# Performance work log

Measured on AMD Instinct MI355X. Metric: run time of the kernel, lower is better.

## Reference

```python
import math
import jax, jax.numpy as jnp
import numpy as np

H = 1024        # hidden_size
NH = 16         # num_attention_heads
HD = H // NH    # attention_head_size
I = 4096        # intermediate_size
B, S = 4, 2048
LN_EPS = 1e-5


def setup_inputs() -> dict:
    key = jax.random.key(0)
    ks = jax.random.split(key, 12)
    s = 0.02
    return {
        "x": jax.random.normal(ks[0], (B, S, H), dtype=jnp.float32),
        "ln1_g": jnp.ones((H,), jnp.float32),
        "ln1_b": jnp.zeros((H,), jnp.float32),
        "qkv_w": jax.random.normal(ks[1], (H, 3 * H), jnp.float32) * s,
        "qkv_b": jnp.zeros((3 * H,), jnp.float32),
        "out_w": jax.random.normal(ks[2], (H, H), jnp.float32) * s,
        "out_b": jnp.zeros((H,), jnp.float32),
        "ln2_g": jnp.ones((H,), jnp.float32),
        "ln2_b": jnp.zeros((H,), jnp.float32),
        "w1": jax.random.normal(ks[3], (H, I), jnp.float32) * s,
        "b1": jnp.zeros((I,), jnp.float32),
        "w2": jax.random.normal(ks[4], (I, H), jnp.float32) * s,
        "b2": jnp.zeros((H,), jnp.float32),
    }


def _layernorm(x, g, b):
    mu = jnp.mean(x, axis=-1, keepdims=True)
    var = jnp.mean(jnp.square(x - mu), axis=-1, keepdims=True)
    return (x - mu) * jax.lax.rsqrt(var + LN_EPS) * g + b


def _gelu_tanh(x):
    c = math.sqrt(2.0 / math.pi)
    return 0.5 * x * (1.0 + jnp.tanh(c * (x + 0.044715 * x * x * x)))


def reference(x, ln1_g, ln1_b, qkv_w, qkv_b, out_w, out_b, ln2_g, ln2_b, w1, b1, w2, b2):
    b, s, _ = x.shape
    h = _layernorm(x, ln1_g, ln1_b)
    qkv = h @ qkv_w + qkv_b                      # [B,S,3H]
    q, k, v = jnp.split(qkv, 3, axis=-1)
    # [B,S,H] -> [B,NH,S,HD]
    def heads(t):
        return t.reshape(b, s, NH, HD).transpose(0, 2, 1, 3)
    q, k, v = heads(q), heads(k), heads(v)
    scores = jnp.einsum("bhqd,bhkd->bhqk", q, k) / math.sqrt(HD)
    probs = jax.nn.softmax(scores, axis=-1)
    attn = jnp.einsum("bhqk,bhkd->bhqd", probs, v)
    attn = attn.transpose(0, 2, 1, 3).reshape(b, s, H)
    attn = attn @ out_w + out_b
    x = x + attn
    h2 = _layernorm(x, ln2_g, ln2_b)
    mlp = _gelu_tanh(h2 @ w1 + b1) @ w2 + b2
    x = x + mlp
    return x
```

## Files before the change

### kernel.cpp

```cpp
#include <hip/hip_runtime.h>
#include <math.h>

#define H 1024
#define NHEAD 16
#define HDIM 64
#define IDIM 4096
#define BATCH 4
#define SEQ 2048
#define NTOK 8192
#define LN_EPS 1e-5f

typedef __bf16 bf16x8 __attribute__((ext_vector_type(8)));
typedef __bf16 bf16x4 __attribute__((ext_vector_type(4)));
typedef float f32x4 __attribute__((ext_vector_type(4)));
typedef unsigned short ushort8 __attribute__((ext_vector_type(8)));
typedef unsigned short ushort4v __attribute__((ext_vector_type(4)));

__device__ __forceinline__ unsigned short f2bf(float f) {
  union { float f; unsigned int u; } v; v.f = f;
  unsigned int u = v.u;
  return (unsigned short)((u + 0x7FFFu + ((u >> 16) & 1u)) >> 16);
}

__global__ void transpose_cast_kernel(const float* __restrict__ W,
                                      unsigned short* __restrict__ Wt,
                                      int K, int N) {
  __shared__ unsigned short tile[32][33];
  int n0 = blockIdx.x * 32, k0 = blockIdx.y * 32;
  int tx = threadIdx.x, ty = threadIdx.y;
#pragma unroll
  for (int i = 0; i < 4; i++) {
    int k = ty + i * 8;
    tile[tx][k] = f2bf(W[(size_t)(k0 + k) * N + n0 + tx]);
  }
  __syncthreads();
#pragma unroll
  for (int i = 0; i < 4; i++) {
    int n = ty + i * 8;
    Wt[(size_t)(n0 + n) * K + k0 + tx] = tile[n][tx];
  }
}

__global__ void transpose_v_kernel(const unsigned short* __restrict__ qkv,
                                   unsigned short* __restrict__ vt) {
  __shared__ unsigned short tile[32][33];
  int s0 = blockIdx.x * 32, d0 = blockIdx.y * 32;
  int bh = blockIdx.z, b = bh >> 4, h = bh & 15;
  int tx = threadIdx.x, ty = threadIdx.y;
#pragma unroll
  for (int i = 0; i < 4; i++) {
    int s = ty + i * 8;
    tile[s][tx] = qkv[((size_t)b * SEQ + s0 + s) * (3 * H) + 2 * H + h * HDIM + d0 + tx];
  }
  __syncthreads();
#pragma unroll
  for (int i = 0; i < 4; i++) {
    int d = ty + i * 8;
    vt[((size_t)bh * HDIM + d0 + d) * SEQ + s0 + tx] = tile[tx][d];
  }
}

__global__ __launch_bounds__(256)
void layernorm_kernel(const float* __restrict__ x, const float* __restrict__ g,
                      const float* __restrict__ b, unsigned short* __restrict__ out) {
  __shared__ float sb[4];
  int row = blockIdx.x;
  int tid = threadIdx.x;
  const float4* xr = (const float4*)(x + (size_t)row * H);
  float4 v = xr[tid];
  float s = v.x + v.y + v.z + v.w;
#pragma unroll
  for (int o = 32; o > 0; o >>= 1) s += __shfl_down(s, o);
  if ((tid & 63) == 0) sb[tid >> 6] = s;
  __syncthreads();
  float mu = (sb[0] + sb[1] + sb[2] + sb[3]) * (1.0f / H);
  __syncthreads();
  float dx = v.x - mu, dy = v.y - mu, dz = v.z - mu, dw = v.w - mu;
  float s2 = dx * dx + dy * dy + dz * dz + dw * dw;
#pragma unroll
  for (int o = 32; o > 0; o >>= 1) s2 += __shfl_down(s2, o);
  if ((tid & 63) == 0) sb[tid >> 6] = s2;
  __syncthreads();
  float var = (sb[0] + sb[1] + sb[2] + sb[3]) * (1.0f / H);
  float rs = rsqrtf(var + LN_EPS);
  float4 gv = ((const float4*)g)[tid];
  float4 bv = ((const float4*)b)[tid];
  ushort4v ov;
  ov[0] = f2bf(dx * rs * gv.x + bv.x);
  ov[1] = f2bf(dy * rs * gv.y + bv.y);
  ov[2] = f2bf(dz * rs * gv.z + bv.z);
  ov[3] = f2bf(dw * rs * gv.w + bv.w);
  ((ushort4v*)(out + (size_t)row * H))[tid] = ov;
}

template <int EPI>
__global__ __launch_bounds__(256)
void gemm_bt_kernel(const unsigned short* __restrict__ A,
                    const unsigned short* __restrict__ Bt,
                    const float* __restrict__ bias,
                    const float* __restrict__ res,
                    void* __restrict__ out, int M, int N, int K) {
  __shared__ __align__(16) unsigned short As[128 * 32];
  __shared__ __align__(16) unsigned short Bs[128 * 32];
  int tid = threadIdx.x;
  int wave = tid >> 6, lane = tid & 63;
  int quad = lane >> 4, l16 = lane & 15;
  int wm = wave >> 1, wn = wave & 1;
  int m0 = blockIdx.y * 128, n0 = blockIdx.x * 128;
  f32x4 acc[4][4];
#pragma unroll
  for (int i = 0; i < 4; i++)
#pragma unroll
    for (int j = 0; j < 4; j++) acc[i][j] = (f32x4){0.f, 0.f, 0.f, 0.f};

  int rl = (lane >> 2);
  int cphys = lane & 3;
  for (int k0 = 0; k0 < K; k0 += 32) {
    __syncthreads();
#pragma unroll
    for (int t = 0; t < 2; t++) {
      int ch = wave * 2 + t;
      int rloc = ch * 16 + rl;
      int clog = cphys ^ ((rloc >> 1) & 3);
      const unsigned short* ga = A + (size_t)(m0 + rloc) * K + k0 + clog * 8;
      __builtin_amdgcn_global_load_lds(
          (const __attribute__((address_space(1))) unsigned int*)ga,
          (__attribute__((address_space(3))) unsigned int*)(As + ch * 512), 16, 0, 0);
      const unsigned short* gb = Bt + (size_t)(n0 + rloc) * K + k0 + clog * 8;
      __builtin_amdgcn_global_load_lds(
          (const __attribute__((address_space(1))) unsigned int*)gb,
          (__attribute__((address_space(3))) unsigned int*)(Bs + ch * 512), 16, 0, 0);
    }
    __syncthreads();
    bf16x8 af[4], bfv[4];
#pragma unroll
    for (int i = 0; i < 4; i++) {
      int ra = wm * 64 + i * 16 + l16;
      af[i] = *(const bf16x8*)&As[ra * 32 + ((quad ^ ((ra >> 1) & 3)) << 3)];
      int rb = wn * 64 + i * 16 + l16;
      bfv[i] = *(const bf16x8*)&Bs[rb * 32 + ((quad ^ ((rb >> 1) & 3)) << 3)];
    }
#pragma unroll
    for (int i = 0; i < 4; i++)
#pragma unroll
      for (int j = 0; j < 4; j++)
        acc[i][j] = __builtin_amdgcn_mfma_f32_16x16x32_bf16(bfv[j], af[i], acc[i][j], 0, 0, 0);
  }
#pragma unroll
  for (int i = 0; i < 4; i++) {
    int m = m0 + wm * 64 + i * 16 + l16;
#pragma unroll
    for (int j = 0; j < 4; j++) {
      int nb = n0 + wn * 64 + j * 16 + quad * 4;
      float4 bv4 = *(const float4*)&bias[nb];
      float v0 = acc[i][j][0] + bv4.x;
      float v1 = acc[i][j][1] + bv4.y;
      float v2 = acc[i][j][2] + bv4.z;
      float v3 = acc[i][j][3] + bv4.w;
      size_t off = (size_t)m * N + nb;
      if (EPI == 0) {
        bf16x4 pk = {(__bf16)v0, (__bf16)v1, (__bf16)v2, (__bf16)v3};
        *(bf16x4*)&((unsigned short*)out)[off] = pk;
      } else if (EPI == 1) {
        float g0 = v0 / (1.f + __expf(-1.5957691216057308f * (v0 + 0.044715f * v0 * v0 * v0)));
        float g1 = v1 / (1.f + __expf(-1.5957691216057308f * (v1 + 0.044715f * v1 * v1 * v1)));
        float g2 = v2 / (1.f + __expf(-1.5957691216057308f * (v2 + 0.044715f * v2 * v2 * v2)));
        float g3 = v3 / (1.f + __expf(-1.5957691216057308f * (v3 + 0.044715f * v3 * v3 * v3)));
        bf16x4 pk = {(__bf16)g0, (__bf16)g1, (__bf16)g2, (__bf16)g3};
        *(bf16x4*)&((unsigned short*)out)[off] = pk;
      } else {
        float4 rv = *(const float4*)&res[off];
        float4 o4;
        o4.x = v0 + rv.x; o4.y = v1 + rv.y; o4.z = v2 + rv.z; o4.w = v3 + rv.w;
        *(float4*)&((float*)out)[off] = o4;
      }
    }
  }
}

__global__ __launch_bounds__(256)
void flash_attn_kernel(const unsigned short* __restrict__ qkv,
                       const unsigned short* __restrict__ vt,
                       unsigned short* __restrict__ attn_out) {
  constexpr int LPs = 72;
  __shared__ __align__(16) unsigned short Ks[64 * 64];
  __shared__ __align__(16) unsigned short Ps[4 * 32 * LPs];
  int tid = threadIdx.x;
  int wave = tid >> 6, lane = tid & 63;
  int quad = lane >> 4, l16 = lane & 15;
  int bh = blockIdx.y, b = bh >> 4, h = bh & 15;
  int qblk = blockIdx.x * 128 + wave * 32;
  const size_t qrow = 3 * H;
  const size_t tok0 = (size_t)b * SEQ;
  const size_t vbase = (size_t)bh * HDIM * SEQ;
  unsigned short* Psw = Ps + wave * 32 * LPs;

  bf16x8 qb[2][2];
#pragma unroll
  for (int mb = 0; mb < 2; mb++)
#pragma unroll
    for (int ks = 0; ks < 2; ks++)
      qb[mb][ks] = *(const bf16x8*)&qkv[(tok0 + qblk + mb * 16 + l16) * qrow +
                                        h * HDIM + ks * 32 + quad * 8];

  float l_part[2] = {0.f, 0.f};
  f32x4 o_acc[2][4];
#pragma unroll
  for (int mb = 0; mb < 2; mb++)
#pragma unroll
    for (int db = 0; db < 4; db++) o_acc[mb][db] = (f32x4){0.f, 0.f, 0.f, 0.f};

  int srow = lane >> 3;
  int schunk = (lane & 7) ^ srow;

  for (int kv0 = 0; kv0 < SEQ; kv0 += 64) {
    __syncthreads();
#pragma unroll
    for (int t = 0; t < 2; t++) {
      int rbase = wave * 16 + t * 8;
      const unsigned short* ga =
          &qkv[(tok0 + kv0 + rbase + srow) * qrow + H + h * HDIM + schunk * 8];
      __builtin_amdgcn_global_load_lds(
          (const __attribute__((address_space(1))) unsigned int*)ga,
          (__attribute__((address_space(3))) unsigned int*)(Ks + rbase * 64), 16, 0, 0);
    }
    bf16x8 va[4][2];
#pragma unroll
    for (int db = 0; db < 4; db++)
#pragma unroll
      for (int ks = 0; ks < 2; ks++)
        va[db][ks] = *(const bf16x8*)&vt[vbase + (size_t)(db * 16 + l16) * SEQ +
                                         kv0 + ks * 32 + quad * 8];
    __syncthreads();
#pragma unroll
    for (int nb = 0; nb < 4; nb++) {
      int row = nb * 16 + l16;
      bf16x8 ka[2];
#pragma unroll
      for (int ks = 0; ks < 2; ks++) {
        int pc = (ks * 4 + quad) ^ (row & 7);
        ka[ks] = *(const bf16x8*)&Ks[row * 64 + pc * 8];
      }
      f32x4 st[2];
#pragma unroll
      for (int mb = 0; mb < 2; mb++) st[mb] = (f32x4){0.f, 0.f, 0.f, 0.f};
#pragma unroll
      for (int ks = 0; ks < 2; ks++)
#pragma unroll
        for (int mb = 0; mb < 2; mb++)
          st[mb] = __builtin_amdgcn_mfma_f32_16x16x32_bf16(ka[ks], qb[mb][ks], st[mb], 0, 0, 0);
#pragma unroll
      for (int mb = 0; mb < 2; mb++) {
        float p0 = __expf(st[mb][0] * 0.125f);
        float p1 = __expf(st[mb][1] * 0.125f);
        float p2 = __expf(st[mb][2] * 0.125f);
        float p3 = __expf(st[mb][3] * 0.125f);
        l_part[mb] += (p0 + p1) + (p2 + p3);
        bf16x4 pk = {(__bf16)p0, (__bf16)p1, (__bf16)p2, (__bf16)p3};
        *(bf16x4*)&Psw[(mb * 16 + l16) * LPs + nb * 16 + quad * 4] = pk;
      }
    }
    __asm__ volatile("s_waitcnt lgkmcnt(0)" ::: "memory");
#pragma unroll
    for (int ks = 0; ks < 2; ks++) {
      bf16x8 pb[2];
#pragma unroll
      for (int mb = 0; mb < 2; mb++)
        pb[mb] = *(const bf16x8*)&Psw[(mb * 16 + l16) * LPs + ks * 32 + quad * 8];
#pragma unroll
      for (int db = 0; db < 4; db++)
#pragma unroll
        for (int mb = 0; mb < 2; mb++)
          o_acc[mb][db] = __builtin_amdgcn_mfma_f32_16x16x32_bf16(va[db][ks], pb[mb],
                                                                  o_acc[mb][db], 0, 0, 0);
    }
  }
#pragma unroll
  for (int mb = 0; mb < 2; mb++) {
    l_part[mb] += __shfl_xor(l_part[mb], 16);
    l_part[mb] += __shfl_xor(l_part[mb], 32);
    l_part[mb] = 1.0f / l_part[mb];
  }
#pragma unroll
  for (int mb = 0; mb < 2; mb++) {
#pragma unroll
    for (int db = 0; db < 4; db++) {
      ushort4v o;
#pragma unroll
      for (int r = 0; r < 4; r++) o[r] = f2bf(o_acc[mb][db][r] * l_part[mb]);
      *(ushort4v*)&attn_out[(tok0 + qblk + mb * 16 + l16) * H + h * HDIM +
                            db * 16 + quad * 4] = o;
    }
  }
}

extern "C" void kernel_launch(void* const* d_in, const int* in_sizes, int n_in,
                              void* d_out, int out_size, void* d_ws, size_t ws_size,
                              hipStream_t stream) {
  const float* x = (const float*)d_in[0];
  const float* ln1_g = (const float*)d_in[1];
  const float* ln1_b = (const float*)d_in[2];
  const float* qkv_w = (const float*)d_in[3];
  const float* qkv_b = (const float*)d_in[4];
  const float* out_w = (const float*)d_in[5];
  const float* out_b = (const float*)d_in[6];
  const float* ln2_g = (const float*)d_in[7];
  const float* ln2_b = (const float*)d_in[8];
  const float* w1 = (const float*)d_in[9];
  const float* b1 = (const float*)d_in[10];
  const float* w2 = (const float*)d_in[11];
  const float* b2 = (const float*)d_in[12];
  float* outp = (float*)d_out;

  size_t off = 0;
  auto take = [&](size_t n) {
    char* p = (char*)d_ws + off;
    off += (n + 255) & ~(size_t)255;
    return p;
  };
  unsigned short* h1 = (unsigned short*)take((size_t)NTOK * H * 2);
  unsigned short* qkvb = (unsigned short*)take((size_t)NTOK * 3 * H * 2);
  unsigned short* attn = (unsigned short*)take((size_t)NTOK * H * 2);
  float* x1 = (float*)take((size_t)NTOK * H * 4);
  unsigned short* qkvwt = (unsigned short*)take((size_t)3 * H * H * 2);
  unsigned short* outwt = (unsigned short*)take((size_t)H * H * 2);
  unsigned short* w1t = (unsigned short*)take((size_t)H * IDIM * 2);
  unsigned short* w2t = (unsigned short*)take((size_t)H * IDIM * 2);
  unsigned short* h2 = h1;
  unsigned short* mid = qkvb;
  unsigned short* vt = (unsigned short*)x1;

  dim3 tb(32, 8);
  transpose_cast_kernel<<<dim3(3 * H / 32, H / 32), tb, 0, stream>>>(qkv_w, qkvwt, H, 3 * H);
  transpose_cast_kernel<<<dim3(H / 32, H / 32), tb, 0, stream>>>(out_w, outwt, H, H);
  transpose_cast_kernel<<<dim3(IDIM / 32, H / 32), tb, 0, stream>>>(w1, w1t, H, IDIM);
  transpose_cast_kernel<<<dim3(H / 32, IDIM / 32), tb, 0, stream>>>(w2, w2t, IDIM, H);

  layernorm_kernel<<<NTOK, 256, 0, stream>>>(x, ln1_g, ln1_b, h1);
  gemm_bt_kernel<0><<<dim3(3 * H / 128, NTOK / 128), 256, 0, stream>>>(
      h1, qkvwt, qkv_b, nullptr, qkvb, NTOK, 3 * H, H);
  transpose_v_kernel<<<dim3(SEQ / 32, HDIM / 32, BATCH * NHEAD), tb, 0, stream>>>(qkvb, vt);
  flash_attn_kernel<<<dim3(SEQ / 128, BATCH * NHEAD), 256, 0, stream>>>(qkvb, vt, attn);
  gemm_bt_kernel<2><<<dim3(H / 128, NTOK / 128), 256, 0, stream>>>(
      attn, outwt, out_b, x, x1, NTOK, H, H);
  layernorm_kernel<<<NTOK, 256, 0, stream>>>(x1, ln2_g, ln2_b, h2);
  gemm_bt_kernel<1><<<dim3(IDIM / 128, NTOK / 128), 256, 0, stream>>>(
      h2, w1t, b1, nullptr, mid, NTOK, IDIM, H);
  gemm_bt_kernel<2><<<dim3(H / 128, NTOK / 128), 256, 0, stream>>>(
      mid, w2t, b2, x1, outp, NTOK, H, IDIM);
}
```

Before: 696.4 us.

## Fuse V transpose into QKV GEMM epilogue and double-buffer K tiles in attention

The QKV GEMM epilogue now writes the V slice straight into the transposed per-head layout, so the separate transpose_v kernel and its extra read and write of V go away. The flash attention kernel double-buffers its K tiles in LDS, prefetching the next tile with async global-to-LDS loads while the current one is computed, and drops one barrier per iteration. It also splits the P·V step into two halves interleaved with the score computation. In exchange, the V epilogue issues scattered 2-byte stores with a stride of SEQ, and the attention kernel uses twice the K shared memory.

```diff
diff --git a/kernel.cpp b/kernel.cpp
--- a/kernel.cpp
+++ b/kernel.cpp
@@ -38,25 +38,6 @@
   for (int i = 0; i < 4; i++) {
     int n = ty + i * 8;
     Wt[(size_t)(n0 + n) * K + k0 + tx] = tile[n][tx];
-  }
-}
-
-__global__ void transpose_v_kernel(const unsigned short* __restrict__ qkv,
-                                   unsigned short* __restrict__ vt) {
-  __shared__ unsigned short tile[32][33];
-  int s0 = blockIdx.x * 32, d0 = blockIdx.y * 32;
-  int bh = blockIdx.z, b = bh >> 4, h = bh & 15;
-  int tx = threadIdx.x, ty = threadIdx.y;
-#pragma unroll
-  for (int i = 0; i < 4; i++) {
-    int s = ty + i * 8;
-    tile[s][tx] = qkv[((size_t)b * SEQ + s0 + s) * (3 * H) + 2 * H + h * HDIM + d0 + tx];
-  }
-  __syncthreads();
-#pragma unroll
-  for (int i = 0; i < 4; i++) {
-    int d = ty + i * 8;
-    vt[((size_t)bh * HDIM + d0 + d) * SEQ + s0 + tx] = tile[tx][d];
   }
 }
 
@@ -99,7 +80,8 @@
                     const unsigned short* __restrict__ Bt,
                     const float* __restrict__ bias,
                     const float* __restrict__ res,
-                    void* __restrict__ out, int M, int N, int K) {
+                    void* __restrict__ out, unsigned short* __restrict__ vt_out,
+                    int M, int N, int K) {
   __shared__ __align__(16) unsigned short As[128 * 32];
   __shared__ __align__(16) unsigned short Bs[128 * 32];
   int tid = threadIdx.x;
@@ -146,6 +128,7 @@
       for (int j = 0; j < 4; j++)
         acc[i][j] = __builtin_amdgcn_mfma_f32_16x16x32_bf16(bfv[j], af[i], acc[i][j], 0, 0, 0);
   }
+  bool vslice = (EPI == 0) && (vt_out != nullptr) && (n0 >= 2 * H);
 #pragma unroll
   for (int i = 0; i < 4; i++) {
     int m = m0 + wm * 64 + i * 16 + l16;
@@ -159,8 +142,19 @@
       float v3 = acc[i][j][3] + bv4.w;
       size_t off = (size_t)m * N + nb;
       if (EPI == 0) {
-        bf16x4 pk = {(__bf16)v0, (__bf16)v1, (__bf16)v2, (__bf16)v3};
-        *(bf16x4*)&((unsigned short*)out)[off] = pk;
+        if (vslice) {
+          int bb = m >> 11, s = m & (SEQ - 1);
+          int cb = nb - 2 * H;
+          int hh = cb >> 6, dd = cb & 63;
+          size_t base = ((size_t)(bb * NHEAD + hh) * HDIM + dd) * SEQ + s;
+          vt_out[base] = f2bf(v0);
+          vt_out[base + SEQ] = f2bf(v1);
+          vt_out[base + 2 * SEQ] = f2bf(v2);
+          vt_out[base + 3 * SEQ] = f2bf(v3);
+        } else {
+          bf16x4 pk = {(__bf16)v0, (__bf16)v1, (__bf16)v2, (__bf16)v3};
+          *(bf16x4*)&((unsigned short*)out)[off] = pk;
+        }
       } else if (EPI == 1) {
         float g0 = v0 / (1.f + __expf(-1.5957691216057308f * (v0 + 0.044715f * v0 * v0 * v0)));
         float g1 = v1 / (1.f + __expf(-1.5957691216057308f * (v1 + 0.044715f * v1 * v1 * v1)));
@@ -183,7 +177,7 @@
                        const unsigned short* __restrict__ vt,
                        unsigned short* __restrict__ attn_out) {
   constexpr int LPs = 72;
-  __shared__ __align__(16) unsigned short Ks[64 * 64];
+  __shared__ __align__(16) unsigned short Ks[2][64 * 64];
   __shared__ __align__(16) unsigned short Ps[4 * 32 * LPs];
   int tid = threadIdx.x;
   int wave = tid >> 6, lane = tid & 63;
@@ -213,17 +207,21 @@
   int srow = lane >> 3;
   int schunk = (lane & 7) ^ srow;
 
+#pragma unroll
+  for (int t = 0; t < 2; t++) {
+    int rbase = wave * 16 + t * 8;
+    const unsigned short* ga =
+        &qkv[(tok0 + rbase + srow) * qrow + H + h * HDIM + schunk * 8];
+    __builtin_amdgcn_global_load_lds(
+        (const __attribute__((address_space(1))) unsigned int*)ga,
+        (__attribute__((address_space(3))) unsigned int*)(&Ks[0][rbase * 64]), 16, 0, 0);
+  }
+
   for (int kv0 = 0; kv0 < SEQ; kv0 += 64) {
+    int buf = (kv0 >> 6) & 1;
+    const unsigned short* Kb = Ks[buf];
+    unsigned short* Kn = Ks[buf ^ 1];
     __syncthreads();
-#pragma unroll
-    for (int t = 0; t < 2; t++) {
-      int rbase = wave * 16 + t * 8;
-      const unsigned short* ga =
-          &qkv[(tok0 + kv0 + rbase + srow) * qrow + H + h * HDIM + schunk * 8];
-      __builtin_amdgcn_global_load_lds(
-          (const __attribute__((address_space(1))) unsigned int*)ga,
-          (__attribute__((address_space(3))) unsigned int*)(Ks + rbase * 64), 16, 0, 0);
-    }
     bf16x8 va[4][2];
 #pragma unroll
     for (int db = 0; db < 4; db++)
@@ -231,47 +229,58 @@
       for (int ks = 0; ks < 2; ks++)
         va[db][ks] = *(const bf16x8*)&vt[vbase + (size_t)(db * 16 + l16) * SEQ +
                                          kv0 + ks * 32 + quad * 8];
-    __syncthreads();
-#pragma unroll
-    for (int nb = 0; nb < 4; nb++) {
-      int row = nb * 16 + l16;
-      bf16x8 ka[2];
-#pragma unroll
-      for (int ks = 0; ks < 2; ks++) {
-        int pc = (ks * 4 + quad) ^ (row & 7);
-        ka[ks] = *(const bf16x8*)&Ks[row * 64 + pc * 8];
+    if (kv0 + 64 < SEQ) {
+#pragma unroll
+      for (int t = 0; t < 2; t++) {
+        int rbase = wave * 16 + t * 8;
+        const unsigned short* ga =
+            &qkv[(tok0 + kv0 + 64 + rbase + srow) * qrow + H + h * HDIM + schunk * 8];
+        __builtin_amdgcn_global_load_lds(
+            (const __attribute__((address_space(1))) unsigned int*)ga,
+            (__attribute__((address_space(3))) unsigned int*)(Kn + rbase * 64), 16, 0, 0);
       }
-      f32x4 st[2];
-#pragma unroll
-      for (int mb = 0; mb < 2; mb++) st[mb] = (f32x4){0.f, 0.f, 0.f, 0.f};
-#pragma unroll
-      for (int ks = 0; ks < 2; ks++)
+    }
+#pragma unroll
+    for (int half = 0; half < 2; half++) {
+#pragma unroll
+      for (int nbl = 0; nbl < 2; nbl++) {
+        int nb = half * 2 + nbl;
+        int row = nb * 16 + l16;
+        bf16x8 ka[2];
+#pragma unroll
+        for (int ks = 0; ks < 2; ks++) {
+          int pc = (ks * 4 + quad) ^ (row & 7);
+          ka[ks] = *(const bf16x8*)&Kb[row * 64 + pc * 8];
+        }
+        f32x4 st[2];
+#pragma unroll
+        for (int mb = 0; mb < 2; mb++) st[mb] = (f32x4){0.f, 0.f, 0.f, 0.f};
+#pragma unroll
+        for (int ks = 0; ks < 2; ks++)
+#pragma unroll
+          for (int mb = 0; mb < 2; mb++)
+            st[mb] = __builtin_amdgcn_mfma_f32_16x16x32_bf16(ka[ks], qb[mb][ks], st[mb], 0, 0, 0);
+#pragma unroll
+        for (int mb = 0; mb < 2; mb++) {
+          float p0 = __expf(st[mb][0] * 0.125f);
+          float p1 = __expf(st[mb][1] * 0.125f);
+          float p2 = __expf(st[mb][2] * 0.125f);
+          float p3 = __expf(st[mb][3] * 0.125f);
+          l_part[mb] += (p0 + p1) + (p2 + p3);
+          bf16x4 pk = {(__bf16)p0, (__bf16)p1, (__bf16)p2, (__bf16)p3};
+          *(bf16x4*)&Psw[(mb * 16 + l16) * LPs + nb * 16 + quad * 4] = pk;
+        }
+      }
+      __asm__ volatile("s_waitcnt lgkmcnt(0)" ::: "memory");
+      bf16x8 pb[2];
+#pragma unroll
+      for (int mb = 0; mb < 2; mb++)
+        pb[mb] = *(const bf16x8*)&Psw[(mb * 16 + l16) * LPs + half * 32 + quad * 8];
+#pragma unroll
+      for (int db = 0; db < 4; db++)
 #pragma unroll
         for (int mb = 0; mb < 2; mb++)
-          st[mb] = __builtin_amdgcn_mfma_f32_16x16x32_bf16(ka[ks], qb[mb][ks], st[mb], 0, 0, 0);
-#pragma unroll
-      for (int mb = 0; mb < 2; mb++) {
-        float p0 = __expf(st[mb][0] * 0.125f);
-        float p1 = __expf(st[mb][1] * 0.125f);
-        float p2 = __expf(st[mb][2] * 0.125f);
-        float p3 = __expf(st[mb][3] * 0.125f);
-        l_part[mb] += (p0 + p1) + (p2 + p3);
-        bf16x4 pk = {(__bf16)p0, (__bf16)p1, (__bf16)p2, (__bf16)p3};
-        *(bf16x4*)&Psw[(mb * 16 + l16) * LPs + nb * 16 + quad * 4] = pk;
-      }
-    }
-    __asm__ volatile("s_waitcnt lgkmcnt(0)" ::: "memory");
-#pragma unroll
-    for (int ks = 0; ks < 2; ks++) {
-      bf16x8 pb[2];
-#pragma unroll
-      for (int mb = 0; mb < 2; mb++)
-        pb[mb] = *(const bf16x8*)&Psw[(mb * 16 + l16) * LPs + ks * 32 + quad * 8];
-#pragma unroll
-      for (int db = 0; db < 4; db++)
-#pragma unroll
-        for (int mb = 0; mb < 2; mb++)
-          o_acc[mb][db] = __builtin_amdgcn_mfma_f32_16x16x32_bf16(va[db][ks], pb[mb],
+          o_acc[mb][db] = __builtin_amdgcn_mfma_f32_16x16x32_bf16(va[db][half], pb[mb],
                                                                   o_acc[mb][db], 0, 0, 0);
     }
   }
@@ -338,14 +347,13 @@
 
   layernorm_kernel<<<NTOK, 256, 0, stream>>>(x, ln1_g, ln1_b, h1);
   gemm_bt_kernel<0><<<dim3(3 * H / 128, NTOK / 128), 256, 0, stream>>>(
-      h1, qkvwt, qkv_b, nullptr, qkvb, NTOK, 3 * H, H);
-  transpose_v_kernel<<<dim3(SEQ / 32, HDIM / 32, BATCH * NHEAD), tb, 0, stream>>>(qkvb, vt);
+      h1, qkvwt, qkv_b, nullptr, qkvb, vt, NTOK, 3 * H, H);
   flash_attn_kernel<<<dim3(SEQ / 128, BATCH * NHEAD), 256, 0, stream>>>(qkvb, vt, attn);
   gemm_bt_kernel<2><<<dim3(H / 128, NTOK / 128), 256, 0, stream>>>(
-      attn, outwt, out_b, x, x1, NTOK, H, H);
+      attn, outwt, out_b, x, x1, nullptr, NTOK, H, H);
   layernorm_kernel<<<NTOK, 256, 0, stream>>>(x1, ln2_g, ln2_b, h2);
   gemm_bt_kernel<1><<<dim3(IDIM / 128, NTOK / 128), 256, 0, stream>>>(
-      h2, w1t, b1, nullptr, mid, NTOK, IDIM, H);
+      h2, w1t, b1, nullptr, mid, nullptr, NTOK, IDIM, H);
   gemm_bt_kernel<2><<<dim3(H / 128, NTOK / 128), 256, 0, stream>>>(
-      mid, w2t, b2, x1, outp, NTOK, H, IDIM);
-}
+      mid, w2t, b2, x1, outp, nullptr, NTOK, H, IDIM);
+}
```

Result: no change. 686.0 us (-1.5%).
